# Kernel optimization log

Hardware: AMD Instinct MI355X
Metric: run time of the kernel (lower is better)

Reference implementation:

```python
import jax, jax.numpy as jnp
import numpy as np

K = 3          # opt.k: number of nearest SOM nodes each point is assigned to
SOM_M = 256    # opt.node_num (16x16 SOM grid)


def _point_resnet(x, ws, bs):
    # SO-Net PointResNet: stack of 1x1 conv (relu) layers; the LAST layer takes
    # concat(prev_out, input) as a residual skip connection.
    out = x
    n = len(ws)
    for i in range(n):
        inp = jnp.concatenate([out, x], axis=1) if i == n - 1 else out
        out = jax.nn.relu(jnp.einsum('oc,bcn->bon', ws[i], inp) + bs[i][None, :, None])
    return out


def _encoder(x, sn, node, fp_ws, fp_bs, fn_ws, fn_bs):
    B, _, N = x.shape
    M = node.shape[2]
    xd = jax.lax.stop_gradient(x)      # torch used x.data throughout SOM logic
    nd = jax.lax.stop_gradient(node)
    # squared distances point->node: B,N,M
    x2 = jnp.sum(xd * xd, axis=1)
    n2 = jnp.sum(nd * nd, axis=1)
    cross = jnp.einsum('bcn,bcm->bnm', xd, nd)
    d2 = x2[:, :, None] + n2[:, None, :] - 2.0 * cross
    _, knn_idx = jax.lax.top_k(-d2, K)                 # B,N,K nearest SOM nodes
    min_idx = jnp.transpose(knn_idx, (0, 2, 1)).reshape(B, K * N)  # B,kN (k-major, matches x_stack)
    x_stack = jnp.tile(x, (1, 1, K))                   # B,3,kN
    xs_d = jax.lax.stop_gradient(x_stack)
    # mask_row_sum (counts per node) and masked sum == one-hot mask multiply in the original
    counts = jax.vmap(lambda s: jax.ops.segment_sum(jnp.ones(s.shape, jnp.float32), s, num_segments=SOM_M))(min_idx)  # B,M
    sums = jax.vmap(lambda d, s: jax.ops.segment_sum(d, s, num_segments=SOM_M))(jnp.transpose(xs_d, (0, 2, 1)), min_idx)  # B,M,3
    cluster_mean = jnp.transpose(sums, (0, 2, 1)) / (counts[:, None, :] + 1e-5)  # B,3,M (new som_node)
    # centers: per-point gather of its assigned node (sum(mask*node) over M)
    centers = jnp.take_along_axis(cluster_mean, min_idx[:, None, :], axis=2)     # B,3,kN
    x_dec = jax.lax.stop_gradient(x_stack - centers)   # .detach() in original
    first = _point_resnet(x_dec, fp_ws, fp_bs)         # B,384,kN
    # index_max + gather: per (b,c,node) max over assigned points; empty nodes -> point index 0
    node_max = jax.vmap(lambda d, s: jax.ops.segment_max(d, s, num_segments=SOM_M))(jnp.transpose(first, (0, 2, 1)), min_idx)  # B,M,C
    node_max = jnp.transpose(node_max, (0, 2, 1))      # B,C,M
    has_pts = counts > 0                               # mask_row_max
    fallback = first[:, :, 0:1]                        # gather index 0 for empty nodes
    masked_max = jnp.where(has_pts[:, None, :], node_max, fallback)  # B,384,M
    final_in = jnp.concatenate([cluster_mean, masked_max], axis=1)   # B,387,M
    final = _point_resnet(final_in, fn_ws, fn_bs)      # B,1024,M
    return jnp.max(final, axis=2)                      # B,1024 global feature


def setup_inputs() -> dict:
    key = jax.random.key(0)
    ks = jax.random.split(key, 24)
    B, N, M = 8, 4096, SOM_M
    inp = {
        'x': jax.random.normal(ks[0], (B, 3, N), jnp.float32),
        'sn': jax.random.normal(ks[1], (B, 3, N), jnp.float32),
        'node': jax.random.normal(ks[2], (B, 3, M), jnp.float32),
        'node_knn_I': jax.random.randint(ks[3], (B, M, 1), 0, M),
    }
    fp_dims = [(3, 64), (64, 128), (128, 256), (256 + 3, 384)]
    fn_dims = [(387, 512), (512, 512), (512, 768), (768 + 387, 1024)]
    i = 4
    for j, (cin, cout) in enumerate(fp_dims):
        inp[f'fp_w{j}'] = jax.random.normal(ks[i], (cout, cin), jnp.float32) * np.float32(np.sqrt(2.0 / cin)); i += 1
        inp[f'fp_b{j}'] = jnp.zeros((cout,), jnp.float32)
    for j, (cin, cout) in enumerate(fn_dims):
        inp[f'fn_w{j}'] = jax.random.normal(ks[i], (cout, cin), jnp.float32) * np.float32(np.sqrt(2.0 / cin)); i += 1
        inp[f'fn_b{j}'] = jnp.zeros((cout,), jnp.float32)
    return inp


def reference(x, sn, node, node_knn_I,
              fp_w0, fp_b0, fp_w1, fp_b1, fp_w2, fp_b2, fp_w3, fp_b3,
              fn_w0, fn_b0, fn_w1, fn_b1, fn_w2, fn_b2, fn_w3, fn_b3):
    fp_ws = [fp_w0, fp_w1, fp_w2, fp_w3]
    fp_bs = [fp_b0, fp_b1, fp_b2, fp_b3]
    fn_ws = [fn_w0, fn_w1, fn_w2, fn_w3]
    fn_bs = [fn_b0, fn_b1, fn_b2, fn_b3]
    # node_knn_I only used when som_k >= 2 (KNNModule); som_k=1 here.
    return _encoder(x, sn, node, fp_ws, fp_bs, fn_ws, fn_bs)
```

## Files before the change

kernel.cpp:

```cpp
#include <hip/hip_runtime.h>
#include <math.h>

#define B_   8
#define N_   4096
#define M_   256
#define KNN_ 3

#define OFF_COUNTS   0
#define OFF_SUMS     8192
#define ZERO_COUNT   32768
#define OFF_CM       32768
#define OFF_NODEMAX  38912
#define OFF_H0       38912
#define OFF_FIRST0   825344
#define OFF_KNN      828416
#define OFF_CATB     828416
#define OFF_SORTED   926720
#define OFF_MSORT    1025024
#define OFF_FIN2     1614848
#define OFF_H1       2040832
#define OFF_WBF      2565120
#define OFF_W3X      3682304
#define O_W0 0
#define O_W1 2048
#define O_W2 10240
#define O_W3 43008
#define O_V0 153600
#define O_V1 366592
#define O_V2 628736
#define O_V3 1021952
#define W_TOTAL 2234368

typedef short  bf16x8 __attribute__((ext_vector_type(8)));
typedef float  f32x4  __attribute__((ext_vector_type(4)));
typedef float  f32x16 __attribute__((ext_vector_type(16)));

__device__ __forceinline__ unsigned short f2b(float f) {
    unsigned u = __float_as_uint(f);
    return (unsigned short)((u + 0x7FFFu + ((u >> 16) & 1u)) >> 16);
}
__device__ __forceinline__ unsigned cvt2(float lo, float hi) {
    unsigned r;
    asm("v_cvt_pk_bf16_f32 %0, %1, %2" : "=v"(r) : "v"(lo), "v"(hi));
    return r;
}
__device__ __forceinline__ f32x16 zero16() {
    f32x16 z;
    #pragma unroll
    for (int i = 0; i < 16; i++) z[i] = 0.f;
    return z;
}

__global__ __launch_bounds__(256) void knn_setup(
        const float* __restrict__ x, const float* __restrict__ node,
        int* __restrict__ knn, float* __restrict__ counts, float* __restrict__ sums,
        const float* s0, const float* s1, const float* s2, const float* s3,
        const float* s4, const float* s5, const float* s6, const float* s7,
        unsigned short* __restrict__ dst, float* __restrict__ w3x) {
    __shared__ float nd0[M_], nd1[M_], nd2[M_], nn2[M_];
    int t = threadIdx.x;
    if (blockIdx.x < 128) {
        int b = blockIdx.x >> 4, xblk = blockIdx.x & 15;
        int rep = blockIdx.x & 3;
        {
            float c0 = node[(b * 3 + 0) * M_ + t];
            float c1 = node[(b * 3 + 1) * M_ + t];
            float c2 = node[(b * 3 + 2) * M_ + t];
            nd0[t] = c0; nd1[t] = c1; nd2[t] = c2;
            nn2[t] = c0 * c0 + c1 * c1 + c2 * c2;
        }
        __syncthreads();
        int n = xblk * 256 + t;
        float x0 = x[(b * 3 + 0) * N_ + n];
        float x1 = x[(b * 3 + 1) * N_ + n];
        float x2 = x[(b * 3 + 2) * N_ + n];
        float xx = x0 * x0 + x1 * x1 + x2 * x2;
        float d0 = 1e30f, d1 = 1e30f, d2b = 1e30f;
        int i0 = 0, i1 = 0, i2 = 0;
        for (int m = 0; m < M_; m++) {
            float cross = x0 * nd0[m] + x1 * nd1[m] + x2 * nd2[m];
            float d = xx + nn2[m] - 2.f * cross;
            bool c0 = d < d0, c1 = d < d1, c2 = d < d2b;
            d2b = c1 ? d1 : (c2 ? d : d2b);
            i2  = c1 ? i1 : (c2 ? m : i2);
            d1  = c0 ? d0 : (c1 ? d : d1);
            i1  = c0 ? i0 : (c1 ? m : i1);
            d0  = c0 ? d  : d0;
            i0  = c0 ? m  : i0;
        }
        int base = (b * N_ + n) * 3;
        knn[base + 0] = i0; knn[base + 1] = i1; knn[base + 2] = i2;
        float* cnt = counts + rep * 2048;
        float* sm  = sums + rep * 6144;
        int mm[3] = {i0, i1, i2};
        #pragma unroll
        for (int k = 0; k < 3; k++) {
            int m = mm[k];
            atomicAdd(&cnt[b * M_ + m], 1.f);
            atomicAdd(&sm[(b * M_ + m) * 3 + 0], x0);
            atomicAdd(&sm[(b * M_ + m) * 3 + 1], x1);
            atomicAdd(&sm[(b * M_ + m) * 3 + 2], x2);
        }
    } else {
        int i = (blockIdx.x - 128) * 256 + t;
        int st = (gridDim.x - 128) * 256;
        for (int j = i; j < 1536; j += st) {
            int ch = j >> 2, c = j & 3;
            w3x[j] = (c < 3) ? s3[ch * 259 + 256 + c] : 0.f;
        }
        for (; i < W_TOTAL; i += st) {
            unsigned short v;
            if (i < O_W1) {
                int loc = i, co = loc >> 5, k = loc & 31;
                v = (k < 3) ? f2b(s0[co * 3 + k]) : (unsigned short)0;
            } else if (i < O_W2) {
                int loc = i - O_W1, co = loc >> 6, k = loc & 63;
                v = f2b(s1[co * 64 + k]);
            } else if (i < O_W3) {
                int loc = i - O_W2, co = loc >> 7, k = loc & 127;
                v = f2b(s2[co * 128 + k]);
            } else if (i < O_V0) {
                int loc = i - O_W3, co = loc / 288u, k = loc - co * 288;
                v = (k < 259) ? f2b(s3[co * 259 + k]) : (unsigned short)0;
            } else if (i < O_V1) {
                int loc = i - O_V0, co = loc / 416u, k = loc - co * 416;
                v = (k < 387) ? f2b(s4[co * 387 + k]) : (unsigned short)0;
            } else if (i < O_V2) {
                int loc = i - O_V1, co = loc >> 9, k = loc & 511;
                v = f2b(s5[co * 512 + k]);
            } else if (i < O_V3) {
                int loc = i - O_V2, co = loc >> 9, k = loc & 511;
                v = f2b(s6[co * 512 + k]);
            } else {
                int loc = i - O_V3, co = loc / 1184u, k = loc - co * 1184;
                v = (k < 1155) ? f2b(s7[co * 1155 + k]) : (unsigned short)0;
            }
            dst[i] = v;
        }
    }
}

__global__ __launch_bounds__(256) void prep(float* __restrict__ counts,
        const float* __restrict__ sums, const int* __restrict__ knn,
        float* __restrict__ cm, int* __restrict__ sorted, int* __restrict__ msort) {
    __shared__ int tmp[256], offsL[257], cur[256];
    int t = threadIdx.x, b = blockIdx.x;
    float cnt = 0.f, s0 = 0.f, s1 = 0.f, s2 = 0.f;
    #pragma unroll
    for (int rp = 0; rp < 4; rp++) {
        cnt += counts[rp * 2048 + b * M_ + t];
        s0 += sums[rp * 6144 + (b * M_ + t) * 3 + 0];
        s1 += sums[rp * 6144 + (b * M_ + t) * 3 + 1];
        s2 += sums[rp * 6144 + (b * M_ + t) * 3 + 2];
    }
    counts[b * M_ + t] = cnt;
    float inv = 1.f / (cnt + 1e-5f);
    cm[(b * 3 + 0) * M_ + t] = s0 * inv;
    cm[(b * 3 + 1) * M_ + t] = s1 * inv;
    cm[(b * 3 + 2) * M_ + t] = s2 * inv;
    int v = (int)cnt;
    tmp[t] = v; cur[t] = 0;
    __syncthreads();
    for (int off = 1; off < 256; off <<= 1) {
        int u = (t >= off) ? tmp[t - off] : 0;
        __syncthreads();
        tmp[t] += u;
        __syncthreads();
    }
    offsL[t] = tmp[t] - v;
    if (t == 255) offsL[256] = tmp[255];
    __syncthreads();
    for (int e = t; e < KNN_ * N_; e += 256) {
        int n = e & (N_ - 1), k = e >> 12;
        int m = knn[(b * N_ + n) * 3 + k];
        int pos = atomicAdd(&cur[m], 1);
        int dst = offsL[m] + pos;
        sorted[b * (KNN_ * N_) + dst] = e;
        msort[b * (KNN_ * N_) + dst] = m;
    }
}

template<int KS, int INS, int OUTS, int CTW>
__device__ __forceinline__ void layerB(const unsigned short* __restrict__ Wg,
        const float* __restrict__ bias, const unsigned short* actin,
        unsigned short* actout, int wave, int lane) {
    int r = lane & 15, g = lane >> 4;
    bf16x8 bfr[4][KS];
    #pragma unroll
    for (int pt = 0; pt < 4; pt++) {
        const unsigned short* arow = actin + (pt * 16 + r) * INS + g * 8;
        #pragma unroll
        for (int ks = 0; ks < KS; ks++)
            bfr[pt][ks] = *(const bf16x8*)(arow + ks * 32);
    }
    #pragma unroll
    for (int c = 0; c < CTW; c++) {
        int ct = wave * CTW + c;
        const unsigned short* wrow = Wg + (ct * 16 + r) * (KS * 32) + g * 8;
        f32x4 acc[4];
        #pragma unroll
        for (int pt = 0; pt < 4; pt++) acc[pt] = (f32x4){0.f, 0.f, 0.f, 0.f};
        #pragma unroll
        for (int ks = 0; ks < KS; ks++) {
            bf16x8 wv = *(const bf16x8*)(wrow + ks * 32);
            #pragma unroll
            for (int pt = 0; pt < 4; pt++)
                acc[pt] = __builtin_amdgcn_mfma_f32_16x16x32_bf16(wv, bfr[pt][ks], acc[pt], 0, 0, 0);
        }
        f32x4 b4 = *(const f32x4*)(bias + ct * 16 + g * 4);
        #pragma unroll
        for (int pt = 0; pt < 4; pt++) {
            uint2 s;
            s.x = cvt2(fmaxf(acc[pt][0] + b4[0], 0.f), fmaxf(acc[pt][1] + b4[1], 0.f));
            s.y = cvt2(fmaxf(acc[pt][2] + b4[2], 0.f), fmaxf(acc[pt][3] + b4[3], 0.f));
            *(uint2*)(actout + (pt * 16 + r) * OUTS + ct * 16 + g * 4) = s;
        }
    }
}

__global__ __launch_bounds__(256, 3) void mlp1m(
        const float* __restrict__ x, const float* __restrict__ cm,
        const int* __restrict__ sorted, const int* __restrict__ msort,
        const unsigned short* __restrict__ wb, const float4* __restrict__ w3x,
        const float* __restrict__ bb0, const float* __restrict__ bb1,
        const float* __restrict__ bb2, const float* __restrict__ bb3,
        float* __restrict__ node_max, float* __restrict__ first0) {
    __shared__ __align__(16) char smem[50688];
    unsigned short* inb = (unsigned short*)smem;
    unsigned short* a1  = (unsigned short*)smem;
    unsigned short* a0  = (unsigned short*)(smem + 16896);
    unsigned short* cat = (unsigned short*)(smem + 16896);
    __shared__ float4 xdf[64];
    __shared__ int segm[65], segstart[66];
    __shared__ int nseg, p0loc;
    int t = threadIdx.x, b = blockIdx.y, lane = t & 63, wave = t >> 6;
    int e0 = blockIdx.x * 64;
    for (int e = t; e < 1280; e += 256) ((unsigned*)inb)[e] = 0u;
    __syncthreads();
    if (t < 64) {
        int p = t;
        if (p == 0) p0loc = -1;
        int j = sorted[b * 12288 + e0 + p];
        int m = msort[b * 12288 + e0 + p];
        int n = j & (N_ - 1);
        float xd0 = x[(b * 3 + 0) * N_ + n] - cm[(b * 3 + 0) * M_ + m];
        float xd1 = x[(b * 3 + 1) * N_ + n] - cm[(b * 3 + 1) * M_ + m];
        float xd2 = x[(b * 3 + 2) * N_ + n] - cm[(b * 3 + 2) * M_ + m];
        xdf[p] = make_float4(xd0, xd1, xd2, 0.f);
        inb[p * 40 + 0] = f2b(xd0);
        inb[p * 40 + 1] = f2b(xd1);
        inb[p * 40 + 2] = f2b(xd2);
        int prev = __shfl_up(m, 1);
        bool flag = (p == 0) || (m != prev);
        unsigned long long mk = __ballot(flag);
        int sid = __popcll(mk & ((1ull << p) - 1ull));
        if (flag) { segstart[sid] = p; segm[sid] = m; }
        if (p == 63) { int ns2 = __popcll(mk); nseg = ns2; segstart[ns2] = 64; }
        if (j == 0) p0loc = p;
    }
    __syncthreads();
    layerB<1, 40, 72, 1>(wb + O_W0, bb0, inb, a0, wave, lane);
    __syncthreads();
    layerB<2, 72, 132, 2>(wb + O_W1, bb1, a0, a1, wave, lane);
    __syncthreads();
    layerB<4, 132, 264, 4>(wb + O_W2, bb2, a1, cat, wave, lane);
    __syncthreads();
    int l31 = lane & 31, half = lane >> 5;
    f32x16 acc[6];
    #pragma unroll
    for (int q = 0; q < 6; q++) acc[q] = zero16();
    {
        const unsigned short* arow0 = cat + l31 * 264 + half * 8;
        const unsigned short* arow1 = cat + (32 + l31) * 264 + half * 8;
        const unsigned short* wrowb = wb + O_W3 + (wave * 96 + l31) * 288 + half * 8;
        #pragma unroll
        for (int ks = 0; ks < 16; ks++) {
            bf16x8 aA = *(const bf16x8*)(arow0 + ks * 16);
            bf16x8 aB = *(const bf16x8*)(arow1 + ks * 16);
            #pragma unroll
            for (int c3 = 0; c3 < 3; c3++) {
                bf16x8 wv = *(const bf16x8*)(wrowb + c3 * 32 * 288 + ks * 16);
                acc[c3 * 2 + 0] = __builtin_amdgcn_mfma_f32_32x32x16_bf16(aA, wv, acc[c3 * 2 + 0], 0, 0, 0);
                acc[c3 * 2 + 1] = __builtin_amdgcn_mfma_f32_32x32x16_bf16(aB, wv, acc[c3 * 2 + 1], 0, 0, 0);
            }
        }
    }
    int ns = nseg, p0l = p0loc;
    float bias3[3]; float4 wx3[3];
    #pragma unroll
    for (int c3 = 0; c3 < 3; c3++) {
        bias3[c3] = bb3[(wave * 3 + c3) * 32 + l31];
        wx3[c3]   = w3x[(wave * 3 + c3) * 32 + l31];
    }
    #pragma unroll
    for (int ph = 0; ph < 2; ph++) {
        #pragma unroll
        for (int rg = 0; rg < 16; rg++) {
            int row = ph * 32 + (rg & 3) + 8 * (rg >> 2) + 4 * half;
            float4 xv = xdf[row];
            #pragma unroll
            for (int c3 = 0; c3 < 3; c3++) {
                float s = acc[c3 * 2 + ph][rg] + bias3[c3]
                        + wx3[c3].x * xv.x + wx3[c3].y * xv.y + wx3[c3].z * xv.z;
                acc[c3 * 2 + ph][rg] = fmaxf(s, 0.f);
            }
        }
    }
    if (p0l >= 0) {
        #pragma unroll
        for (int ph = 0; ph < 2; ph++)
            #pragma unroll
            for (int rg = 0; rg < 16; rg++) {
                int row = ph * 32 + (rg & 3) + 8 * (rg >> 2) + 4 * half;
                if (row == p0l) {
                    #pragma unroll
                    for (int c3 = 0; c3 < 3; c3++)
                        first0[b * 384 + (wave * 3 + c3) * 32 + l31] = acc[c3 * 2 + ph][rg];
                }
            }
    }
    for (int s = 0; s < ns; s++) {
        int s0 = segstart[s], s1 = segstart[s + 1];
        float m0 = 0.f, m1 = 0.f, m2 = 0.f;
        if (s0 < 32) {
            #pragma unroll
            for (int rg = 0; rg < 16; rg++) {
                int row = (rg & 3) + 8 * (rg >> 2) + 4 * half;
                bool in = (row >= s0) && (row < s1);
                m0 = fmaxf(m0, in ? acc[0][rg] : 0.f);
                m1 = fmaxf(m1, in ? acc[2][rg] : 0.f);
                m2 = fmaxf(m2, in ? acc[4][rg] : 0.f);
            }
        }
        if (s1 > 32) {
            #pragma unroll
            for (int rg = 0; rg < 16; rg++) {
                int row = 32 + (rg & 3) + 8 * (rg >> 2) + 4 * half;
                bool in = (row >= s0) && (row < s1);
                m0 = fmaxf(m0, in ? acc[1][rg] : 0.f);
                m1 = fmaxf(m1, in ? acc[3][rg] : 0.f);
                m2 = fmaxf(m2, in ? acc[5][rg] : 0.f);
            }
        }
        m0 = fmaxf(m0, __shfl_xor(m0, 32));
        m1 = fmaxf(m1, __shfl_xor(m1, 32));
        m2 = fmaxf(m2, __shfl_xor(m2, 32));
        if (lane < 32) {
            float* dstp = &node_max[(size_t)(b * M_ + segm[s]) * 384 + wave * 96];
            atomicMax((int*)(dstp + l31),      __float_as_int(m0));
            atomicMax((int*)(dstp + 32 + l31), __float_as_int(m1));
            atomicMax((int*)(dstp + 64 + l31), __float_as_int(m2));
        }
    }
}

__global__ void build_fin2(const float* __restrict__ cm, const float* __restrict__ counts,
                           const float* __restrict__ nmax, const float* __restrict__ first0,
                           unsigned short* __restrict__ fin2) {
    int tot = 2048 * 416;
    int i = blockIdx.x * blockDim.x + threadIdx.x;
    int st = gridDim.x * blockDim.x;
    for (; i < tot; i += st) {
        int n = i / 416, ch = i - n * 416;
        int b = n >> 8, m = n & 255;
        float v = 0.f;
        if (ch < 3) v = cm[(b * 3 + ch) * M_ + m];
        else if (ch < 387)
            v = (counts[n] > 0.f) ? nmax[(size_t)n * 384 + (ch - 3)]
                                  : first0[b * 384 + (ch - 3)];
        fin2[n * 416 + ch] = f2b(v);
    }
}

template<int KS, int CTQ>
__global__ __launch_bounds__(256, 2) void nlayer4(const unsigned short* __restrict__ W,
        const float* __restrict__ bias, const unsigned short* __restrict__ actin,
        unsigned short* __restrict__ actout, int outs) {
    int wave = threadIdx.x >> 6, lane = threadIdx.x & 63;
    int id = blockIdx.x * 4 + wave;
    int nt = id / CTQ, cq = id - nt * CTQ;
    int r = lane & 15, g = lane >> 4;
    const unsigned short* arow = actin + (size_t)(nt * 16 + r) * (KS * 32) + g * 8;
    bf16x8 afr[KS];
    #pragma unroll
    for (int ks = 0; ks < KS; ks++) afr[ks] = *(const bf16x8*)(arow + ks * 32);
    const unsigned short* w0 = W + (cq * 64 + r) * (KS * 32) + g * 8;
    f32x4 acc[4];
    #pragma unroll
    for (int c = 0; c < 4; c++) acc[c] = (f32x4){0.f, 0.f, 0.f, 0.f};
    #pragma unroll
    for (int ks = 0; ks < KS; ks++) {
        #pragma unroll
        for (int c = 0; c < 4; c++) {
            bf16x8 wv = *(const bf16x8*)(w0 + c * 16 * KS * 32 + ks * 32);
            acc[c] = __builtin_amdgcn_mfma_f32_16x16x32_bf16(wv, afr[ks], acc[c], 0, 0, 0);
        }
    }
    #pragma unroll
    for (int c = 0; c < 4; c++) {
        f32x4 b4 = *(const f32x4*)(bias + cq * 64 + c * 16 + g * 4);
        uint2 s;
        s.x = cvt2(fmaxf(acc[c][0] + b4[0], 0.f), fmaxf(acc[c][1] + b4[1], 0.f));
        s.y = cvt2(fmaxf(acc[c][2] + b4[2], 0.f), fmaxf(acc[c][3] + b4[3], 0.f));
        *(uint2*)(actout + (size_t)(nt * 16 + r) * outs + cq * 64 + c * 16 + g * 4) = s;
    }
}

__global__ __launch_bounds__(256) void nlayer_max_s(const unsigned short* __restrict__ W,
        const float* __restrict__ bias, const unsigned short* __restrict__ catb,
        const unsigned short* __restrict__ fin2, float* __restrict__ out) {
    int wave = threadIdx.x >> 6, lane = threadIdx.x & 63;
    int id = blockIdx.x * 4 + wave;
    int nt = id >> 5, cp = id & 31;
    int r = lane & 15, g = lane >> 4;
    const unsigned short* arow0 = catb + (size_t)(nt * 16 + r) * 768 + g * 8;
    const unsigned short* arow1 = fin2 + (size_t)(nt * 16 + r) * 416 + g * 8;
    const unsigned short* w0 = W + (size_t)(cp * 32 + r) * 1184 + g * 8;
    const unsigned short* w1 = w0 + 16 * 1184;
    f32x4 a0 = {0.f, 0.f, 0.f, 0.f}, a1 = {0.f, 0.f, 0.f, 0.f};
    #pragma unroll 4
    for (int ks = 0; ks < 24; ks++) {
        bf16x8 av = *(const bf16x8*)(arow0 + ks * 32);
        a0 = __builtin_amdgcn_mfma_f32_16x16x32_bf16(*(const bf16x8*)(w0 + ks * 32), av, a0, 0, 0, 0);
        a1 = __builtin_amdgcn_mfma_f32_16x16x32_bf16(*(const bf16x8*)(w1 + ks * 32), av, a1, 0, 0, 0);
    }
    #pragma unroll 4
    for (int ks = 0; ks < 13; ks++) {
        bf16x8 av = *(const bf16x8*)(arow1 + ks * 32);
        a0 = __builtin_amdgcn_mfma_f32_16x16x32_bf16(*(const bf16x8*)(w0 + (24 + ks) * 32), av, a0, 0, 0, 0);
        a1 = __builtin_amdgcn_mfma_f32_16x16x32_bf16(*(const bf16x8*)(w1 + (24 + ks) * 32), av, a1, 0, 0, 0);
    }
    int b = nt >> 4;
    #pragma unroll
    for (int c = 0; c < 2; c++) {
        f32x4 acc = c ? a1 : a0;
        f32x4 b4 = *(const f32x4*)(bias + cp * 32 + c * 16 + g * 4);
        #pragma unroll
        for (int i = 0; i < 4; i++) {
            float v = fmaxf(acc[i] + b4[i], 0.f);
            v = fmaxf(v, __shfl_xor(v, 1));
            v = fmaxf(v, __shfl_xor(v, 2));
            v = fmaxf(v, __shfl_xor(v, 4));
            v = fmaxf(v, __shfl_xor(v, 8));
            if (r == 0)
                atomicMax((int*)&out[b * 1024 + cp * 32 + c * 16 + g * 4 + i],
                          __float_as_int(v));
        }
    }
}

extern "C" void kernel_launch(void* const* d_in, const int* in_sizes, int n_in,
                              void* d_out, int out_size, void* d_ws, size_t ws_size,
                              hipStream_t stream) {
    (void)in_sizes; (void)n_in; (void)out_size; (void)ws_size;
    const float* x    = (const float*)d_in[0];
    const float* node = (const float*)d_in[2];
    const float* fpw[4] = {(const float*)d_in[4], (const float*)d_in[6],
                           (const float*)d_in[8], (const float*)d_in[10]};
    const float* fpb[4] = {(const float*)d_in[5], (const float*)d_in[7],
                           (const float*)d_in[9], (const float*)d_in[11]};
    const float* fnw[4] = {(const float*)d_in[12], (const float*)d_in[14],
                           (const float*)d_in[16], (const float*)d_in[18]};
    const float* fnb[4] = {(const float*)d_in[13], (const float*)d_in[15],
                           (const float*)d_in[17], (const float*)d_in[19]};
    float* ws  = (float*)d_ws;
    float* out = (float*)d_out;
    unsigned short* wb   = (unsigned short*)(ws + OFF_WBF);
    unsigned short* fin2 = (unsigned short*)(ws + OFF_FIN2);
    unsigned short* h0   = (unsigned short*)(ws + OFF_H0);
    unsigned short* h1   = (unsigned short*)(ws + OFF_H1);
    unsigned short* catb = (unsigned short*)(ws + OFF_CATB);

    hipMemsetAsync(ws, 0, (size_t)ZERO_COUNT * 4, stream);
    hipMemsetAsync(ws + OFF_NODEMAX, 0, (size_t)(B_ * M_ * 384) * 4, stream);

    knn_setup<<<128 + 2048, 256, 0, stream>>>(
        x, node, (int*)(ws + OFF_KNN), ws + OFF_COUNTS, ws + OFF_SUMS,
        fpw[0], fpw[1], fpw[2], fpw[3], fnw[0], fnw[1], fnw[2], fnw[3],
        wb, ws + OFF_W3X);
    prep<<<B_, 256, 0, stream>>>(
        ws + OFF_COUNTS, ws + OFF_SUMS, (int*)(ws + OFF_KNN),
        ws + OFF_CM, (int*)(ws + OFF_SORTED), (int*)(ws + OFF_MSORT));
    mlp1m<<<dim3(KNN_ * N_ / 64, B_), 256, 0, stream>>>(
        x, ws + OFF_CM, (int*)(ws + OFF_SORTED), (int*)(ws + OFF_MSORT), wb,
        (const float4*)(ws + OFF_W3X),
        fpb[0], fpb[1], fpb[2], fpb[3], ws + OFF_NODEMAX, ws + OFF_FIRST0);
    build_fin2<<<3328, 256, 0, stream>>>(
        ws + OFF_CM, ws + OFF_COUNTS, ws + OFF_NODEMAX, ws + OFF_FIRST0, fin2);
    nlayer4<13, 8><<<256,  256, 0, stream>>>(wb + O_V0, fnb[0], fin2, h0, 512);
    nlayer4<16, 8><<<256,  256, 0, stream>>>(wb + O_V1, fnb[1], h0, h1, 512);
    nlayer4<16, 12><<<384, 256, 0, stream>>>(wb + O_V2, fnb[2], h1, catb, 768);
    nlayer_max_s<<<1024, 256, 0, stream>>>(wb + O_V3, fnb[3], catb, fin2, out);
}
```

Before: 196.1 us.

## Fuse tail MLP layers into one persistent kernel with grid barriers

Replaces the build_fin2 kernel and the four node-MLP layer launches with a single 256-block kernel that separates the stages with atomic-counter grid barriers. The barrier counters live in the zeroed workspace region, and the output is now zeroed by an explicit memset. The aim is to remove launch gaps and tail idle time between the five small kernels. In exchange, the later layers run on fewer blocks than before and so get less parallelism, the spin barriers cost time, and the scheme depends on all 256 blocks being resident at once.

```diff
diff --git a/kernel.cpp b/kernel.cpp
--- a/kernel.cpp
+++ b/kernel.cpp
@@ -8,19 +8,20 @@
 
 #define OFF_COUNTS   0
 #define OFF_SUMS     8192
-#define ZERO_COUNT   32768
-#define OFF_CM       32768
-#define OFF_NODEMAX  38912
-#define OFF_H0       38912
-#define OFF_FIRST0   825344
-#define OFF_KNN      828416
-#define OFF_CATB     828416
-#define OFF_SORTED   926720
-#define OFF_MSORT    1025024
-#define OFF_FIN2     1614848
-#define OFF_H1       2040832
-#define OFF_WBF      2565120
-#define OFF_W3X      3682304
+#define OFF_BAR      32768
+#define ZERO_COUNT   32784
+#define OFF_CM       32784
+#define OFF_NODEMAX  38928
+#define OFF_H0       38928
+#define OFF_FIRST0   825360
+#define OFF_KNN      828432
+#define OFF_CATB     828432
+#define OFF_SORTED   926736
+#define OFF_MSORT    1025040
+#define OFF_FIN2     1614864
+#define OFF_H1       2040848
+#define OFF_WBF      2565136
+#define OFF_W3X      3682320
 #define O_W0 0
 #define O_W1 2048
 #define O_W2 10240
@@ -49,6 +50,17 @@
     #pragma unroll
     for (int i = 0; i < 16; i++) z[i] = 0.f;
     return z;
+}
+
+__device__ __forceinline__ void gridbar(int* c, int nblk) {
+    __syncthreads();
+    if (threadIdx.x == 0) {
+        __threadfence();
+        atomicAdd(c, 1);
+        while (atomicAdd(c, 0) < nblk) {}
+        __threadfence();
+    }
+    __syncthreads();
 }
 
 __global__ __launch_bounds__(256) void knn_setup(
@@ -354,37 +366,15 @@
     }
 }
 
-__global__ void build_fin2(const float* __restrict__ cm, const float* __restrict__ counts,
-                           const float* __restrict__ nmax, const float* __restrict__ first0,
-                           unsigned short* __restrict__ fin2) {
-    int tot = 2048 * 416;
-    int i = blockIdx.x * blockDim.x + threadIdx.x;
-    int st = gridDim.x * blockDim.x;
-    for (; i < tot; i += st) {
-        int n = i / 416, ch = i - n * 416;
-        int b = n >> 8, m = n & 255;
-        float v = 0.f;
-        if (ch < 3) v = cm[(b * 3 + ch) * M_ + m];
-        else if (ch < 387)
-            v = (counts[n] > 0.f) ? nmax[(size_t)n * 384 + (ch - 3)]
-                                  : first0[b * 384 + (ch - 3)];
-        fin2[n * 416 + ch] = f2b(v);
-    }
-}
-
-template<int KS, int CTQ>
-__global__ __launch_bounds__(256, 2) void nlayer4(const unsigned short* __restrict__ W,
+template<int KS>
+__device__ __forceinline__ void nbody(const unsigned short* __restrict__ W,
         const float* __restrict__ bias, const unsigned short* __restrict__ actin,
-        unsigned short* __restrict__ actout, int outs) {
-    int wave = threadIdx.x >> 6, lane = threadIdx.x & 63;
-    int id = blockIdx.x * 4 + wave;
-    int nt = id / CTQ, cq = id - nt * CTQ;
-    int r = lane & 15, g = lane >> 4;
+        unsigned short* __restrict__ actout, int outs, int nt, int cq, int r, int g) {
     const unsigned short* arow = actin + (size_t)(nt * 16 + r) * (KS * 32) + g * 8;
     bf16x8 afr[KS];
     #pragma unroll
     for (int ks = 0; ks < KS; ks++) afr[ks] = *(const bf16x8*)(arow + ks * 32);
-    const unsigned short* w0 = W + (cq * 64 + r) * (KS * 32) + g * 8;
+    const unsigned short* w0 = W + (size_t)(cq * 64 + r) * (KS * 32) + g * 8;
     f32x4 acc[4];
     #pragma unroll
     for (int c = 0; c < 4; c++) acc[c] = (f32x4){0.f, 0.f, 0.f, 0.f};
@@ -406,45 +396,83 @@
     }
 }
 
-__global__ __launch_bounds__(256) void nlayer_max_s(const unsigned short* __restrict__ W,
-        const float* __restrict__ bias, const unsigned short* __restrict__ catb,
-        const unsigned short* __restrict__ fin2, float* __restrict__ out) {
-    int wave = threadIdx.x >> 6, lane = threadIdx.x & 63;
-    int id = blockIdx.x * 4 + wave;
-    int nt = id >> 5, cp = id & 31;
+__global__ __launch_bounds__(256) void tail_fused(
+        const float* __restrict__ cm, const float* __restrict__ counts,
+        const float* __restrict__ nmax, const float* __restrict__ first0,
+        const unsigned short* __restrict__ wb,
+        const float* __restrict__ q0, const float* __restrict__ q1,
+        const float* __restrict__ q2, const float* __restrict__ q3,
+        unsigned short* __restrict__ fin2, unsigned short* __restrict__ h0,
+        unsigned short* __restrict__ h1, unsigned short* __restrict__ catb,
+        float* __restrict__ out, int* __restrict__ bar) {
+    int t = threadIdx.x, lane = t & 63, wave = t >> 6;
     int r = lane & 15, g = lane >> 4;
-    const unsigned short* arow0 = catb + (size_t)(nt * 16 + r) * 768 + g * 8;
-    const unsigned short* arow1 = fin2 + (size_t)(nt * 16 + r) * 416 + g * 8;
-    const unsigned short* w0 = W + (size_t)(cp * 32 + r) * 1184 + g * 8;
-    const unsigned short* w1 = w0 + 16 * 1184;
-    f32x4 a0 = {0.f, 0.f, 0.f, 0.f}, a1 = {0.f, 0.f, 0.f, 0.f};
-    #pragma unroll 4
-    for (int ks = 0; ks < 24; ks++) {
-        bf16x8 av = *(const bf16x8*)(arow0 + ks * 32);
-        a0 = __builtin_amdgcn_mfma_f32_16x16x32_bf16(*(const bf16x8*)(w0 + ks * 32), av, a0, 0, 0, 0);
-        a1 = __builtin_amdgcn_mfma_f32_16x16x32_bf16(*(const bf16x8*)(w1 + ks * 32), av, a1, 0, 0, 0);
-    }
-    #pragma unroll 4
-    for (int ks = 0; ks < 13; ks++) {
-        bf16x8 av = *(const bf16x8*)(arow1 + ks * 32);
-        a0 = __builtin_amdgcn_mfma_f32_16x16x32_bf16(*(const bf16x8*)(w0 + (24 + ks) * 32), av, a0, 0, 0, 0);
-        a1 = __builtin_amdgcn_mfma_f32_16x16x32_bf16(*(const bf16x8*)(w1 + (24 + ks) * 32), av, a1, 0, 0, 0);
-    }
-    int b = nt >> 4;
-    #pragma unroll
-    for (int c = 0; c < 2; c++) {
-        f32x4 acc = c ? a1 : a0;
-        f32x4 b4 = *(const f32x4*)(bias + cp * 32 + c * 16 + g * 4);
-        #pragma unroll
-        for (int i = 0; i < 4; i++) {
-            float v = fmaxf(acc[i] + b4[i], 0.f);
-            v = fmaxf(v, __shfl_xor(v, 1));
-            v = fmaxf(v, __shfl_xor(v, 2));
-            v = fmaxf(v, __shfl_xor(v, 4));
-            v = fmaxf(v, __shfl_xor(v, 8));
-            if (r == 0)
-                atomicMax((int*)&out[b * 1024 + cp * 32 + c * 16 + g * 4 + i],
-                          __float_as_int(v));
+    int nblk = gridDim.x;
+    {
+        int i = blockIdx.x * 256 + t;
+        int st = nblk * 256;
+        for (; i < 2048 * 416; i += st) {
+            int n = i / 416, ch = i - n * 416;
+            int b = n >> 8, m = n & 255;
+            float v = 0.f;
+            if (ch < 3) v = cm[(b * 3 + ch) * M_ + m];
+            else if (ch < 387)
+                v = (counts[n] > 0.f) ? nmax[(size_t)n * 384 + (ch - 3)]
+                                      : first0[b * 384 + (ch - 3)];
+            fin2[n * 416 + ch] = f2b(v);
+        }
+    }
+    gridbar(bar + 0, nblk);
+    {
+        int id = blockIdx.x * 4 + wave;
+        nbody<13>(wb + O_V0, q0, fin2, h0, 512, id >> 3, id & 7, r, g);
+    }
+    gridbar(bar + 1, nblk);
+    {
+        int id = blockIdx.x * 4 + wave;
+        nbody<16>(wb + O_V1, q1, h0, h1, 512, id >> 3, id & 7, r, g);
+    }
+    gridbar(bar + 2, nblk);
+    for (int id = blockIdx.x * 4 + wave; id < 1536; id += nblk * 4) {
+        int nt = id / 12, cq = id - nt * 12;
+        nbody<16>(wb + O_V2, q2, h1, catb, 768, nt, cq, r, g);
+    }
+    gridbar(bar + 3, nblk);
+    for (int id = blockIdx.x * 4 + wave; id < 4096; id += nblk * 4) {
+        int nt = id >> 5, cp = id & 31;
+        const unsigned short* arow0 = catb + (size_t)(nt * 16 + r) * 768 + g * 8;
+        const unsigned short* arow1 = fin2 + (size_t)(nt * 16 + r) * 416 + g * 8;
+        const unsigned short* w0 = wb + O_V3 + (size_t)(cp * 32 + r) * 1184 + g * 8;
+        const unsigned short* w1 = w0 + 16 * 1184;
+        f32x4 a0 = {0.f, 0.f, 0.f, 0.f}, a1 = {0.f, 0.f, 0.f, 0.f};
+        #pragma unroll 4
+        for (int ks = 0; ks < 24; ks++) {
+            bf16x8 av = *(const bf16x8*)(arow0 + ks * 32);
+            a0 = __builtin_amdgcn_mfma_f32_16x16x32_bf16(*(const bf16x8*)(w0 + ks * 32), av, a0, 0, 0, 0);
+            a1 = __builtin_amdgcn_mfma_f32_16x16x32_bf16(*(const bf16x8*)(w1 + ks * 32), av, a1, 0, 0, 0);
+        }
+        #pragma unroll 4
+        for (int ks = 0; ks < 13; ks++) {
+            bf16x8 av = *(const bf16x8*)(arow1 + ks * 32);
+            a0 = __builtin_amdgcn_mfma_f32_16x16x32_bf16(*(const bf16x8*)(w0 + (24 + ks) * 32), av, a0, 0, 0, 0);
+            a1 = __builtin_amdgcn_mfma_f32_16x16x32_bf16(*(const bf16x8*)(w1 + (24 + ks) * 32), av, a1, 0, 0, 0);
+        }
+        int b = nt >> 4;
+        #pragma unroll
+        for (int c = 0; c < 2; c++) {
+            f32x4 acc = c ? a1 : a0;
+            f32x4 b4 = *(const f32x4*)((c ? q3 : q3) + cp * 32 + c * 16 + g * 4);
+            #pragma unroll
+            for (int i = 0; i < 4; i++) {
+                float v = fmaxf(acc[i] + b4[i], 0.f);
+                v = fmaxf(v, __shfl_xor(v, 1));
+                v = fmaxf(v, __shfl_xor(v, 2));
+                v = fmaxf(v, __shfl_xor(v, 4));
+                v = fmaxf(v, __shfl_xor(v, 8));
+                if (r == 0)
+                    atomicMax((int*)&out[b * 1024 + cp * 32 + c * 16 + g * 4 + i],
+                              __float_as_int(v));
+            }
         }
     }
 }
@@ -473,6 +501,7 @@
 
     hipMemsetAsync(ws, 0, (size_t)ZERO_COUNT * 4, stream);
     hipMemsetAsync(ws + OFF_NODEMAX, 0, (size_t)(B_ * M_ * 384) * 4, stream);
+    hipMemsetAsync(out, 0, (size_t)B_ * 1024 * 4, stream);
 
     knn_setup<<<128 + 2048, 256, 0, stream>>>(
         x, node, (int*)(ws + OFF_KNN), ws + OFF_COUNTS, ws + OFF_SUMS,
@@ -485,10 +514,8 @@
         x, ws + OFF_CM, (int*)(ws + OFF_SORTED), (int*)(ws + OFF_MSORT), wb,
         (const float4*)(ws + OFF_W3X),
         fpb[0], fpb[1], fpb[2], fpb[3], ws + OFF_NODEMAX, ws + OFF_FIRST0);
-    build_fin2<<<3328, 256, 0, stream>>>(
-        ws + OFF_CM, ws + OFF_COUNTS, ws + OFF_NODEMAX, ws + OFF_FIRST0, fin2);
-    nlayer4<13, 8><<<256,  256, 0, stream>>>(wb + O_V0, fnb[0], fin2, h0, 512);
-    nlayer4<16, 8><<<256,  256, 0, stream>>>(wb + O_V1, fnb[1], h0, h1, 512);
-    nlayer4<16, 12><<<384, 256, 0, stream>>>(wb + O_V2, fnb[2], h1, catb, 768);
-    nlayer_max_s<<<1024, 256, 0, stream>>>(wb + O_V3, fnb[3], catb, fin2, out);
-}
+    tail_fused<<<256, 256, 0, stream>>>(
+        ws + OFF_CM, ws + OFF_COUNTS, ws + OFF_NODEMAX, ws + OFF_FIRST0, wb,
+        fnb[0], fnb[1], fnb[2], fnb[3],
+        fin2, h0, h1, catb, out, (int*)(ws + OFF_BAR));
+}
```

Result: slower. 294.1 us (+50.0%).

## Fuse fin2 construction into first node MLP layer and fold nodemax zeroing into setup

Applied to the files above, without the earlier changes.

Removes the standalone build_fin2 kernel. The first fn layer now builds its 16-row bf16 input tile in LDS from cluster means, node maxima and first0, then runs the MFMA GEMM on it directly. Only one of the two column-half blocks writes fin2 back to global, since the residual last layer still needs it. The hipMemset of the node_max buffer is replaced by extra zeroing blocks inside knn_setup, which cuts a launch and an input-activation round trip. The cost is duplicated gather work across the two column-half blocks. There is also a possible hazard: h0 shares its workspace offset with node_max, so h0 writes could overlap node_max rows still being read by other blocks of the same kernel.

```diff
diff --git a/kernel.cpp b/kernel.cpp
--- a/kernel.cpp
+++ b/kernel.cpp
@@ -56,7 +56,8 @@
         int* __restrict__ knn, float* __restrict__ counts, float* __restrict__ sums,
         const float* s0, const float* s1, const float* s2, const float* s3,
         const float* s4, const float* s5, const float* s6, const float* s7,
-        unsigned short* __restrict__ dst, float* __restrict__ w3x) {
+        unsigned short* __restrict__ dst, float* __restrict__ w3x,
+        float4* __restrict__ nodemax4) {
     __shared__ float nd0[M_], nd1[M_], nd2[M_], nn2[M_];
     int t = threadIdx.x;
     if (blockIdx.x < 128) {
@@ -101,9 +102,14 @@
             atomicAdd(&sm[(b * M_ + m) * 3 + 1], x1);
             atomicAdd(&sm[(b * M_ + m) * 3 + 2], x2);
         }
+    } else if (blockIdx.x < 512) {
+        int i = (blockIdx.x - 128) * 256 + t;
+        int st = 384 * 256;
+        f32x4 z4 = {0.f, 0.f, 0.f, 0.f};
+        for (; i < 196608; i += st) ((f32x4*)nodemax4)[i] = z4;
     } else {
-        int i = (blockIdx.x - 128) * 256 + t;
-        int st = (gridDim.x - 128) * 256;
+        int i = (blockIdx.x - 512) * 256 + t;
+        int st = (gridDim.x - 512) * 256;
         for (int j = i; j < 1536; j += st) {
             int ch = j >> 2, c = j & 3;
             w3x[j] = (c < 3) ? s3[ch * 259 + 256 + c] : 0.f;
@@ -354,21 +360,53 @@
     }
 }
 
-__global__ void build_fin2(const float* __restrict__ cm, const float* __restrict__ counts,
-                           const float* __restrict__ nmax, const float* __restrict__ first0,
-                           unsigned short* __restrict__ fin2) {
-    int tot = 2048 * 416;
-    int i = blockIdx.x * blockDim.x + threadIdx.x;
-    int st = gridDim.x * blockDim.x;
-    for (; i < tot; i += st) {
-        int n = i / 416, ch = i - n * 416;
-        int b = n >> 8, m = n & 255;
+__global__ __launch_bounds__(256, 2) void nlayer0_fin(const unsigned short* __restrict__ W,
+        const float* __restrict__ bias,
+        const float* __restrict__ cm, const float* __restrict__ counts,
+        const float* __restrict__ nmax, const float* __restrict__ first0,
+        unsigned short* __restrict__ fin2, unsigned short* __restrict__ actout) {
+    __shared__ __align__(16) unsigned short finL[16 * 416];
+    int t = threadIdx.x, wave = t >> 6, lane = t & 63;
+    int nt = blockIdx.x >> 1, cq0 = (blockIdx.x & 1) * 4;
+    int b = nt >> 4;
+    for (int e = t; e < 16 * 416; e += 256) {
+        int nl = e / 416, ch = e - nl * 416;
+        int ng = nt * 16 + nl, m = ng & 255;
         float v = 0.f;
         if (ch < 3) v = cm[(b * 3 + ch) * M_ + m];
         else if (ch < 387)
-            v = (counts[n] > 0.f) ? nmax[(size_t)n * 384 + (ch - 3)]
-                                  : first0[b * 384 + (ch - 3)];
-        fin2[n * 416 + ch] = f2b(v);
+            v = (counts[ng] > 0.f) ? nmax[(size_t)ng * 384 + (ch - 3)]
+                                   : first0[b * 384 + (ch - 3)];
+        unsigned short u = f2b(v);
+        finL[e] = u;
+        if (cq0 == 0) fin2[(size_t)ng * 416 + ch] = u;
+    }
+    __syncthreads();
+    int r = lane & 15, g = lane >> 4;
+    int cq = cq0 + wave;
+    const unsigned short* arow = finL + r * 416 + g * 8;
+    bf16x8 afr[13];
+    #pragma unroll
+    for (int ks = 0; ks < 13; ks++) afr[ks] = *(const bf16x8*)(arow + ks * 32);
+    const unsigned short* w0 = W + (size_t)(cq * 64 + r) * 416 + g * 8;
+    f32x4 acc[4];
+    #pragma unroll
+    for (int c = 0; c < 4; c++) acc[c] = (f32x4){0.f, 0.f, 0.f, 0.f};
+    #pragma unroll
+    for (int ks = 0; ks < 13; ks++) {
+        #pragma unroll
+        for (int c = 0; c < 4; c++) {
+            bf16x8 wv = *(const bf16x8*)(w0 + c * 16 * 416 + ks * 32);
+            acc[c] = __builtin_amdgcn_mfma_f32_16x16x32_bf16(wv, afr[ks], acc[c], 0, 0, 0);
+        }
+    }
+    #pragma unroll
+    for (int c = 0; c < 4; c++) {
+        f32x4 b4 = *(const f32x4*)(bias + cq * 64 + c * 16 + g * 4);
+        uint2 s;
+        s.x = cvt2(fmaxf(acc[c][0] + b4[0], 0.f), fmaxf(acc[c][1] + b4[1], 0.f));
+        s.y = cvt2(fmaxf(acc[c][2] + b4[2], 0.f), fmaxf(acc[c][3] + b4[3], 0.f));
+        *(uint2*)(actout + (size_t)(nt * 16 + r) * 512 + cq * 64 + c * 16 + g * 4) = s;
     }
 }
 
@@ -384,7 +422,7 @@
     bf16x8 afr[KS];
     #pragma unroll
     for (int ks = 0; ks < KS; ks++) afr[ks] = *(const bf16x8*)(arow + ks * 32);
-    const unsigned short* w0 = W + (cq * 64 + r) * (KS * 32) + g * 8;
+    const unsigned short* w0 = W + (size_t)(cq * 64 + r) * (KS * 32) + g * 8;
     f32x4 acc[4];
     #pragma unroll
     for (int c = 0; c < 4; c++) acc[c] = (f32x4){0.f, 0.f, 0.f, 0.f};
@@ -472,12 +510,12 @@
     unsigned short* catb = (unsigned short*)(ws + OFF_CATB);
 
     hipMemsetAsync(ws, 0, (size_t)ZERO_COUNT * 4, stream);
-    hipMemsetAsync(ws + OFF_NODEMAX, 0, (size_t)(B_ * M_ * 384) * 4, stream);
-
-    knn_setup<<<128 + 2048, 256, 0, stream>>>(
+    hipMemsetAsync(out, 0, (size_t)B_ * 1024 * 4, stream);
+
+    knn_setup<<<512 + 2048, 256, 0, stream>>>(
         x, node, (int*)(ws + OFF_KNN), ws + OFF_COUNTS, ws + OFF_SUMS,
         fpw[0], fpw[1], fpw[2], fpw[3], fnw[0], fnw[1], fnw[2], fnw[3],
-        wb, ws + OFF_W3X);
+        wb, ws + OFF_W3X, (float4*)(ws + OFF_NODEMAX));
     prep<<<B_, 256, 0, stream>>>(
         ws + OFF_COUNTS, ws + OFF_SUMS, (int*)(ws + OFF_KNN),
         ws + OFF_CM, (int*)(ws + OFF_SORTED), (int*)(ws + OFF_MSORT));
@@ -485,9 +523,9 @@
         x, ws + OFF_CM, (int*)(ws + OFF_SORTED), (int*)(ws + OFF_MSORT), wb,
         (const float4*)(ws + OFF_W3X),
         fpb[0], fpb[1], fpb[2], fpb[3], ws + OFF_NODEMAX, ws + OFF_FIRST0);
-    build_fin2<<<3328, 256, 0, stream>>>(
-        ws + OFF_CM, ws + OFF_COUNTS, ws + OFF_NODEMAX, ws + OFF_FIRST0, fin2);
-    nlayer4<13, 8><<<256,  256, 0, stream>>>(wb + O_V0, fnb[0], fin2, h0, 512);
+    nlayer0_fin<<<256, 256, 0, stream>>>(
+        wb + O_V0, fnb[0], ws + OFF_CM, ws + OFF_COUNTS,
+        ws + OFF_NODEMAX, ws + OFF_FIRST0, fin2, h0);
     nlayer4<16, 8><<<256,  256, 0, stream>>>(wb + O_V1, fnb[1], h0, h1, 512);
     nlayer4<16, 12><<<384, 256, 0, stream>>>(wb + O_V2, fnb[2], h1, catb, 768);
     nlayer_max_s<<<1024, 256, 0, stream>>>(wb + O_V3, fnb[3], catb, fin2, out);
```

Measured after the change: 202.2 us. 1.03x slower.
